# Kernel optimization log

Hardware: AMD Instinct MI355X
Metric: run time of the kernel (lower is better)

The kernel has to match this reference:

```python
import jax, jax.numpy as jnp
import numpy as np

E = 128  # embedding dim (edim)
NEG_INF = -1e8


def setup_inputs() -> dict:
    key = jax.random.key(0)
    ks = jax.random.split(key, 12)
    n_users, n_items, B, L = 100000, 50000, 4096, 64
    s = 1.0 / np.sqrt(2 * E)
    return {
        "user_embs": jax.random.normal(ks[0], (n_users, E), jnp.float32),
        "item_embs": jax.random.normal(ks[1], (n_items, E), jnp.float32),
        "w_uu": jax.random.normal(ks[2], (2 * E,), jnp.float32) * s,
        "w_uiu": jax.random.normal(ks[3], (2 * E,), jnp.float32) * s,
        "w_uui": jax.random.normal(ks[4], (2 * E,), jnp.float32) * s,
        "W0": jax.random.normal(ks[5], (E, E // 2), jnp.float32) / np.sqrt(E),
        "b0": jax.random.normal(ks[6], (E // 2,), jnp.float32) * 0.01,
        "w1": jax.random.normal(ks[7], (E // 2,), jnp.float32) / np.sqrt(E // 2),
        "uid": jax.random.randint(ks[8], (B,), 0, n_users),
        "nbr": jax.random.randint(ks[9], (B, L), 0, n_users),
        "uiu": jax.random.randint(ks[10], (B, 2, L), 0, n_items),
        "uui": jax.random.randint(ks[11], (B, 2, L), 0, n_items),
    }


def reference(user_embs, item_embs, w_uu, w_uiu, w_uui, W0, b0, w1, uid, nbr, uiu, uui):
    self_emb = user_embs[uid][:, None, :]  # [B,1,E]

    def branch(feat, mask, w):
        # feat: [B,L,E], mask: [B,L] bool. concat([self,feat]) @ w split into two GEMVs.
        logits = self_emb @ w[:E, None] + feat @ w[E:, None]  # [B,L,1]
        logits = jax.nn.leaky_relu(logits)  # slope 0.01, matches F.leaky_relu default
        logits = logits + NEG_INF * mask[:, :, None].astype(feat.dtype)
        a = jax.nn.softmax(logits, axis=1)  # over neighbor dim
        return jax.nn.relu(jnp.sum(a * feat, axis=1))  # [B,E]

    # uu meta-path
    uu_feat = branch((self_emb + user_embs[nbr]) * 0.5, nbr == 0, w_uu)
    # uiu meta-path: row 0 = item ids, row 1 = user ids
    mp_iid, mp_uid = uiu[:, 0], uiu[:, 1]
    uiu_feat = branch((self_emb + item_embs[mp_iid] + user_embs[mp_uid]) / 3.0, mp_iid == 0, w_uiu)
    # uui meta-path: row 0 = user ids, row 1 = item ids
    mp_uid2, mp_iid2 = uui[:, 0], uui[:, 1]
    uui_feat = branch((self_emb + user_embs[mp_uid2] + item_embs[mp_iid2]) / 3.0, mp_uid2 == 0, w_uui)

    def inter(feat):
        return jnp.tanh(feat @ W0 + b0).mean(axis=0) @ w1  # scalar

    scores = jnp.stack([inter(uu_feat), inter(uiu_feat), inter(uui_feat)])
    mp = jax.nn.softmax(scores)
    return jax.nn.relu(mp[0] * uu_feat + mp[1] * uiu_feat + mp[2] * uui_feat)
```

## Files before the change

kernel.cpp:

```cpp
#include <hip/hip_runtime.h>
#include <hip/hip_bf16.h>

#define E_DIM 128
#define L_DIM 64
#define HDIM 64

__device__ __forceinline__ float waveSum(float v) {
#pragma unroll
  for (int o = 32; o > 0; o >>= 1) v += __shfl_xor(v, o);
  return v;
}
__device__ __forceinline__ float waveMax(float v) {
#pragma unroll
  for (int o = 32; o > 0; o >>= 1) v = fmaxf(v, __shfl_xor(v, o));
  return v;
}
__device__ __forceinline__ float halfSum(float v) {
#pragma unroll
  for (int o = 16; o > 0; o >>= 1) v += __shfl_xor(v, o);
  return v;
}

__device__ __forceinline__ unsigned int f2bf(float f) {
  unsigned int u = __float_as_uint(f);
  return (u + 0x7fffu + ((u >> 16) & 1u)) >> 16;
}
__device__ __forceinline__ float lo_bf(unsigned int q) {
  return __uint_as_float(q << 16);
}
__device__ __forceinline__ float hi_bf(unsigned int q) {
  return __uint_as_float(q & 0xffff0000u);
}

__global__ __launch_bounds__(256) void convert_all(
    const float* __restrict__ user_src, const float* __restrict__ item_src,
    unsigned short* __restrict__ user_bf, unsigned short* __restrict__ item_bf,
    const float* __restrict__ w_uu, const float* __restrict__ w_uiu,
    const float* __restrict__ w_uui, float* __restrict__ pU0,
    float* __restrict__ pU1, float* __restrict__ pU2,
    float* __restrict__ pI1, float* __restrict__ pI2, int nUr, int nIr) {
  const int lane = threadIdx.x & 63;
  const int j = lane & 31;
  const int h = lane >> 5;
  const int gw = blockIdx.x * 4 + (threadIdx.x >> 6);
  const int r_all = gw * 2 + h;
  if (r_all >= nUr + nIr) return;

  const bool is_user = (r_all < nUr);
  const int r = is_user ? r_all : r_all - nUr;
  const float* src = is_user ? user_src : item_src;
  unsigned short* dst = is_user ? user_bf : item_bf;

  const float4 v = *(const float4*)(src + (long)r * E_DIM + j * 4);
  const unsigned int b0p = f2bf(v.x) | (f2bf(v.y) << 16);
  const unsigned int b1p = f2bf(v.z) | (f2bf(v.w) << 16);
  ((uint2*)dst)[(long)r * (E_DIM / 4) + j] = make_uint2(b0p, b1p);
  const float x0 = lo_bf(b0p), x1 = hi_bf(b0p);
  const float x2 = lo_bf(b1p), x3 = hi_bf(b1p);

  const float* wA = is_user ? w_uu : w_uiu;
  const float* wB = is_user ? w_uiu : w_uui;
  const float4 a4 = *(const float4*)(wA + E_DIM + j * 4);
  const float dA = halfSum(x0 * a4.x + x1 * a4.y + x2 * a4.z + x3 * a4.w);
  const float4 b4 = *(const float4*)(wB + E_DIM + j * 4);
  const float dB = halfSum(x0 * b4.x + x1 * b4.y + x2 * b4.z + x3 * b4.w);
  float dC = 0.f;
  if (is_user) {
    const float4 c4 = *(const float4*)(w_uui + E_DIM + j * 4);
    dC = halfSum(x0 * c4.x + x1 * c4.y + x2 * c4.z + x3 * c4.w);
  }
  if (j == 0) {
    if (is_user) {
      pU0[r] = dA;
      pU1[r] = dB;
      pU2[r] = dC;
    } else {
      pI1[r] = dA;
      pI2[r] = dB;
    }
  }
}

__global__ __launch_bounds__(256) void phase1_proj(
    const float* __restrict__ user_embs,
    const unsigned short* __restrict__ user_bf,
    const unsigned short* __restrict__ item_bf,
    const float* __restrict__ projU0, const float* __restrict__ projU1,
    const float* __restrict__ projU2, const float* __restrict__ projI1,
    const float* __restrict__ projI2,
    const float* __restrict__ w_uu, const float* __restrict__ w_uiu,
    const float* __restrict__ w_uui, const float* __restrict__ W0,
    const float* __restrict__ b0, const float* __restrict__ w1,
    const int* __restrict__ uid, const int* __restrict__ nbr,
    const int* __restrict__ uiu, const int* __restrict__ uui,
    float* __restrict__ feats,
    float* __restrict__ partials,
    int B) {
  const int lane = threadIdx.x & 63;
  const int j = lane & 15;
  const int quarter = lane >> 4;
  const int wv = threadIdx.x >> 6;
  const int w_id = blockIdx.x * 4 + wv;
  const int b = w_id / 3;
  const int k = w_id - 3 * b;
  if (b >= B) return;

  __shared__ float sc[4][E_DIM];

  const int u = uid[b];
  const float2 self2 = *(const float2*)(user_embs + (long)u * E_DIM + lane * 2);

  const float* w = (k == 0) ? w_uu : (k == 1) ? w_uiu : w_uui;
  const float2 wa = *(const float2*)(w + lane * 2);
  const float2 wb = *(const float2*)(w + E_DIM + lane * 2);
  const float S1 = waveSum(self2.x * wa.x + self2.y * wa.y);
  const float S2 = waveSum(self2.x * wb.x + self2.y * wb.y);

  const bool is_uu = (k == 0);
  const float scale = is_uu ? 0.5f : (1.0f / 3.0f);
  const uint4* T0 = (const uint4*)((k == 1) ? item_bf : user_bf);
  const uint4* T1 = (const uint4*)((k == 1) ? user_bf : item_bf);
  const float* p0 = (k == 0) ? projU0 : (k == 1) ? projI1 : projU2;
  const float* p1 = (k == 1) ? projU1 : projI2;

  int i0_l, i1_l;
  if (is_uu) {
    i0_l = nbr[b * L_DIM + lane];
    i1_l = 0;
  } else {
    const int* mp = (k == 1) ? uiu : uui;
    i0_l = mp[(b * 2 + 0) * L_DIM + lane];
    i1_l = mp[(b * 2 + 1) * L_DIM + lane];
  }

  float d = p0[i0_l];
  if (!is_uu) d += p1[i1_l];
  float logit = S1 + scale * (S2 + d);
  logit = (logit > 0.f) ? logit : 0.01f * logit;
  if (i0_l == 0) logit += -100000000.0f;

  const float M = waveMax(logit);
  const float p = __expf(logit - M);
  const float Z = waveSum(p);
  const float a_l = p / Z;

  constexpr int RQ = E_DIM / 8;
  float o0 = 0.f, o1 = 0.f, o2 = 0.f, o3 = 0.f;
  float o4 = 0.f, o5 = 0.f, o6 = 0.f, o7 = 0.f;

  int l4 = quarter;
  float a_cur = __shfl(a_l, l4);
  int i0 = __shfl(i0_l, l4);
  uint4 q0 = T0[(long)i0 * RQ + j];
  uint4 q1 = make_uint4(0, 0, 0, 0);
  if (!is_uu) {
    const int i1 = __shfl(i1_l, l4);
    q1 = T1[(long)i1 * RQ + j];
  }

  for (int it = 0; it < L_DIM / 4; ++it) {
    const float a = a_cur;
    const uint4 qa = q0;
    const uint4 qb = q1;
    if (it < L_DIM / 4 - 1) {
      l4 = 4 * (it + 1) + quarter;
      a_cur = __shfl(a_l, l4);
      i0 = __shfl(i0_l, l4);
      q0 = T0[(long)i0 * RQ + j];
      if (!is_uu) {
        const int i1 = __shfl(i1_l, l4);
        q1 = T1[(long)i1 * RQ + j];
      }
    }
    float h0 = lo_bf(qa.x), h1 = hi_bf(qa.x);
    float h2 = lo_bf(qa.y), h3 = hi_bf(qa.y);
    float h4 = lo_bf(qa.z), h5 = hi_bf(qa.z);
    float h6 = lo_bf(qa.w), h7 = hi_bf(qa.w);
    if (!is_uu) {
      h0 += lo_bf(qb.x); h1 += hi_bf(qb.x);
      h2 += lo_bf(qb.y); h3 += hi_bf(qb.y);
      h4 += lo_bf(qb.z); h5 += hi_bf(qb.z);
      h6 += lo_bf(qb.w); h7 += hi_bf(qb.w);
    }
    o0 += a * h0; o1 += a * h1; o2 += a * h2; o3 += a * h3;
    o4 += a * h4; o5 += a * h5; o6 += a * h6; o7 += a * h7;
  }
  o0 += __shfl_xor(o0, 16); o0 += __shfl_xor(o0, 32);
  o1 += __shfl_xor(o1, 16); o1 += __shfl_xor(o1, 32);
  o2 += __shfl_xor(o2, 16); o2 += __shfl_xor(o2, 32);
  o3 += __shfl_xor(o3, 16); o3 += __shfl_xor(o3, 32);
  o4 += __shfl_xor(o4, 16); o4 += __shfl_xor(o4, 32);
  o5 += __shfl_xor(o5, 16); o5 += __shfl_xor(o5, 32);
  o6 += __shfl_xor(o6, 16); o6 += __shfl_xor(o6, 32);
  o7 += __shfl_xor(o7, 16); o7 += __shfl_xor(o7, 32);

  const float4 sA = *(const float4*)(user_embs + (long)u * E_DIM + j * 8);
  const float4 sB = *(const float4*)(user_embs + (long)u * E_DIM + j * 8 + 4);
  float4 rA, rB;
  rA.x = fmaxf((sA.x + o0) * scale, 0.f);
  rA.y = fmaxf((sA.y + o1) * scale, 0.f);
  rA.z = fmaxf((sA.z + o2) * scale, 0.f);
  rA.w = fmaxf((sA.w + o3) * scale, 0.f);
  rB.x = fmaxf((sB.x + o4) * scale, 0.f);
  rB.y = fmaxf((sB.y + o5) * scale, 0.f);
  rB.z = fmaxf((sB.z + o6) * scale, 0.f);
  rB.w = fmaxf((sB.w + o7) * scale, 0.f);
  if (lane < 16) {
    float* fp = feats + ((long)k * B + b) * E_DIM + j * 8;
    *(float4*)fp = rA;
    *(float4*)(fp + 4) = rB;
    *(float4*)(&sc[wv][j * 8]) = rA;
    *(float4*)(&sc[wv][j * 8 + 4]) = rB;
  }
  __syncthreads();

  float hid = b0[lane];
#pragma unroll 4
  for (int e = 0; e < E_DIM; ++e) hid += sc[wv][e] * W0[e * HDIM + lane];
  const float pp = tanhf(hid) * w1[lane];
  const float sum = waveSum(pp);
  if (lane == 0) partials[(long)k * B + b] = sum;
}

__global__ __launch_bounds__(256) void phase1_f32(
    const float* __restrict__ user_embs, const float* __restrict__ item_embs,
    const float* __restrict__ w_uu, const float* __restrict__ w_uiu,
    const float* __restrict__ w_uui, const float* __restrict__ W0,
    const float* __restrict__ b0, const float* __restrict__ w1,
    const int* __restrict__ uid, const int* __restrict__ nbr,
    const int* __restrict__ uiu, const int* __restrict__ uui,
    float* __restrict__ feats, float* __restrict__ partials, int B) {
  const int lane = threadIdx.x & 63;
  const int wv = threadIdx.x >> 6;
  const int w_id = blockIdx.x * 4 + wv;
  const int b = w_id / 3;
  const int k = w_id - 3 * b;
  if (b >= B) return;

  __shared__ float sc[4][E_DIM];
  const int u = uid[b];
  const float self0 = user_embs[u * E_DIM + lane];
  const float self1 = user_embs[u * E_DIM + 64 + lane];
  const float* w = (k == 0) ? w_uu : (k == 1) ? w_uiu : w_uui;
  const float wa0 = w[lane], wa1 = w[64 + lane];
  const float wb0 = w[128 + lane], wb1 = w[192 + lane];
  const float logit_self = waveSum(self0 * wa0 + self1 * wa1);
  const bool is_uu = (k == 0);
  const float scale = is_uu ? 0.5f : (1.0f / 3.0f);
  const float* t0 = (k == 1) ? item_embs : user_embs;
  const float* t1 = (k == 1) ? user_embs : item_embs;
  int i0_l, i1_l;
  if (is_uu) {
    i0_l = nbr[b * L_DIM + lane];
    i1_l = 0;
  } else {
    const int* mp = (k == 1) ? uiu : uui;
    i0_l = mp[(b * 2 + 0) * L_DIM + lane];
    i1_l = mp[(b * 2 + 1) * L_DIM + lane];
  }
  const float mask_l = (i0_l == 0) ? 1.0f : 0.0f;
  float m = -3.0e38f, s = 0.0f, o0 = 0.0f, o1 = 0.0f;
  int i0 = __shfl(i0_l, 0), i1 = __shfl(i1_l, 0);
  float g00 = t0[i0 * E_DIM + lane];
  float g01 = t0[i0 * E_DIM + 64 + lane];
  float g10 = 0.f, g11 = 0.f;
  if (!is_uu) {
    g10 = t1[i1 * E_DIM + lane];
    g11 = t1[i1 * E_DIM + 64 + lane];
  }
  for (int l = 0; l < L_DIM; ++l) {
    const float f0 = (self0 + g00 + g10) * scale;
    const float f1 = (self1 + g01 + g11) * scale;
    if (l < L_DIM - 1) {
      i0 = __shfl(i0_l, l + 1);
      i1 = __shfl(i1_l, l + 1);
      g00 = t0[i0 * E_DIM + lane];
      g01 = t0[i0 * E_DIM + 64 + lane];
      if (!is_uu) {
        g10 = t1[i1 * E_DIM + lane];
        g11 = t1[i1 * E_DIM + 64 + lane];
      }
    }
    float logit = waveSum(f0 * wb0 + f1 * wb1) + logit_self;
    logit = (logit > 0.f) ? logit : 0.01f * logit;
    logit += -100000000.0f * __shfl(mask_l, l);
    const float mn = fmaxf(m, logit);
    const float alpha = __expf(m - mn);
    const float p = __expf(logit - mn);
    s = s * alpha + p;
    o0 = o0 * alpha + p * f0;
    o1 = o1 * alpha + p * f1;
    m = mn;
  }
  const float inv_s = 1.0f / s;
  const float r0 = fmaxf(o0 * inv_s, 0.f);
  const float r1 = fmaxf(o1 * inv_s, 0.f);
  feats[((long)k * B + b) * E_DIM + lane] = r0;
  feats[((long)k * B + b) * E_DIM + 64 + lane] = r1;
  sc[wv][lane] = r0;
  sc[wv][64 + lane] = r1;
  __syncthreads();
  float hid = b0[lane];
#pragma unroll 4
  for (int e = 0; e < E_DIM; ++e) hid += sc[wv][e] * W0[e * HDIM + lane];
  const float p = tanhf(hid) * w1[lane];
  const float sum = waveSum(p);
  if (lane == 0) partials[(long)k * B + b] = sum;
}

__global__ __launch_bounds__(256) void reduce_scores(
    const float* __restrict__ partials, float* __restrict__ weights, int B) {
  __shared__ float red[256];
  const int tid = threadIdx.x;
  float s[3];
#pragma unroll
  for (int k = 0; k < 3; ++k) {
    float acc = 0.f;
    for (int i = tid; i < B; i += 256) acc += partials[(long)k * B + i];
    red[tid] = acc;
    __syncthreads();
    for (int off = 128; off > 0; off >>= 1) {
      if (tid < off) red[tid] += red[tid + off];
      __syncthreads();
    }
    s[k] = red[0];
    __syncthreads();
  }
  if (tid == 0) {
    const float inv_b = 1.0f / (float)B;
    const float s0 = s[0] * inv_b, s1 = s[1] * inv_b, s2 = s[2] * inv_b;
    const float m = fmaxf(s0, fmaxf(s1, s2));
    const float e0 = __expf(s0 - m);
    const float e1 = __expf(s1 - m);
    const float e2 = __expf(s2 - m);
    const float inv = 1.0f / (e0 + e1 + e2);
    weights[0] = e0 * inv;
    weights[1] = e1 * inv;
    weights[2] = e2 * inv;
  }
}

__global__ __launch_bounds__(256) void phase2(
    const float* __restrict__ feats, const float* __restrict__ weights,
    float* __restrict__ out, int B) {
  const int i = blockIdx.x * blockDim.x + threadIdx.x;
  const int n = B * E_DIM;
  if (i >= n) return;
  const float w0 = weights[0], w1 = weights[1], w2 = weights[2];
  const float v = w0 * feats[i] + w1 * feats[n + i] + w2 * feats[2 * n + i];
  out[i] = fmaxf(v, 0.f);
}

__global__ __launch_bounds__(256) void phase2_fused(
    const float* __restrict__ partials, const float* __restrict__ feats,
    float* __restrict__ out, int B) {
  __shared__ float red[3][4];
  const int tid = threadIdx.x;
  const int lane = tid & 63;
  const int wv = tid >> 6;

  float s0 = 0.f, s1 = 0.f, s2 = 0.f;
  if ((B & 3) == 0) {
    const float4* p4 = (const float4*)partials;
    const int nb4 = B >> 2;
    for (int i = tid; i < nb4; i += 256) {
      const float4 v0 = p4[i];
      const float4 v1 = p4[nb4 + i];
      const float4 v2 = p4[2 * nb4 + i];
      s0 += (v0.x + v0.y) + (v0.z + v0.w);
      s1 += (v1.x + v1.y) + (v1.z + v1.w);
      s2 += (v2.x + v2.y) + (v2.z + v2.w);
    }
  } else {
    for (int i = tid; i < B; i += 256) {
      s0 += partials[i];
      s1 += partials[B + i];
      s2 += partials[2 * B + i];
    }
  }
  s0 = waveSum(s0);
  s1 = waveSum(s1);
  s2 = waveSum(s2);
  if (lane == 0) {
    red[0][wv] = s0;
    red[1][wv] = s1;
    red[2][wv] = s2;
  }
  __syncthreads();
  const float inv_b = 1.0f / (float)B;
  const float a0 = (red[0][0] + red[0][1] + red[0][2] + red[0][3]) * inv_b;
  const float a1 = (red[1][0] + red[1][1] + red[1][2] + red[1][3]) * inv_b;
  const float a2 = (red[2][0] + red[2][1] + red[2][2] + red[2][3]) * inv_b;
  const float m = fmaxf(a0, fmaxf(a1, a2));
  const float e0 = __expf(a0 - m);
  const float e1 = __expf(a1 - m);
  const float e2 = __expf(a2 - m);
  const float inv = 1.0f / (e0 + e1 + e2);
  const float w0 = e0 * inv, w1 = e1 * inv, w2 = e2 * inv;

  const int n4 = (B * E_DIM) >> 2;
  const float4* f4 = (const float4*)feats;
  float4* o4 = (float4*)out;
  for (int i = blockIdx.x * 256 + tid; i < n4; i += gridDim.x * 256) {
    const float4 x = f4[i];
    const float4 y = f4[n4 + i];
    const float4 z = f4[2 * n4 + i];
    float4 r;
    r.x = fmaxf(w0 * x.x + w1 * y.x + w2 * z.x, 0.f);
    r.y = fmaxf(w0 * x.y + w1 * y.y + w2 * z.y, 0.f);
    r.z = fmaxf(w0 * x.z + w1 * y.z + w2 * z.z, 0.f);
    r.w = fmaxf(w0 * x.w + w1 * y.w + w2 * z.w, 0.f);
    o4[i] = r;
  }
}

extern "C" void kernel_launch(void* const* d_in, const int* in_sizes, int n_in,
                              void* d_out, int out_size, void* d_ws,
                              size_t ws_size, hipStream_t stream) {
  const float* user_embs = (const float*)d_in[0];
  const float* item_embs = (const float*)d_in[1];
  const float* w_uu = (const float*)d_in[2];
  const float* w_uiu = (const float*)d_in[3];
  const float* w_uui = (const float*)d_in[4];
  const float* W0 = (const float*)d_in[5];
  const float* b0 = (const float*)d_in[6];
  const float* w1 = (const float*)d_in[7];
  const int* uid = (const int*)d_in[8];
  const int* nbr = (const int*)d_in[9];
  const int* uiu = (const int*)d_in[10];
  const int* uui = (const int*)d_in[11];
  const int B = in_sizes[8];
  const int nU = in_sizes[0];
  const int nI = in_sizes[1];
  const int nUr = nU / E_DIM;
  const int nIr = nI / E_DIM;

  float* ws = (float*)d_ws;
  float* partials = ws;
  float* weights = ws + 3 * B;
  float* feats = ws + 3 * B + 64;
  const size_t f32_floats = (size_t)3 * B + 64 + (size_t)3 * B * E_DIM;
  unsigned short* user_bf = (unsigned short*)(ws + f32_floats);
  unsigned short* item_bf = user_bf + nU;
  float* projU0 = (float*)(item_bf + nI);
  float* projU1 = projU0 + nUr;
  float* projU2 = projU1 + nUr;
  float* projI1 = projU2 + nUr;
  float* projI2 = projI1 + nIr;
  const size_t need = f32_floats * 4 + ((size_t)nU + nI) * 2 +
                      ((size_t)3 * nUr + 2 * nIr) * 4;

  const int n_waves = 3 * B;
  const int n_blocks = (n_waves + 3) / 4;
  const int n = B * E_DIM;

  if (ws_size >= need) {
    const int conv_waves = (nUr + nIr + 1) / 2;
    convert_all<<<(conv_waves + 3) / 4, 256, 0, stream>>>(
        user_embs, item_embs, user_bf, item_bf, w_uu, w_uiu, w_uui, projU0,
        projU1, projU2, projI1, projI2, nUr, nIr);
    phase1_proj<<<n_blocks, 256, 0, stream>>>(
        user_embs, user_bf, item_bf, projU0, projU1, projU2, projI1, projI2,
        w_uu, w_uiu, w_uui, W0, b0, w1, uid, nbr, uiu, uui, feats, partials,
        B);
    phase2_fused<<<256, 256, 0, stream>>>(partials, feats, (float*)d_out, B);
  } else {
    phase1_f32<<<n_blocks, 256, 0, stream>>>(user_embs, item_embs, w_uu,
                                             w_uiu, w_uui, W0, b0, w1, uid,
                                             nbr, uiu, uui, feats, partials, B);
    reduce_scores<<<1, 256, 0, stream>>>(partials, weights, B);
    phase2<<<(n + 255) / 256, 256, 0, stream>>>(feats, weights, (float*)d_out,
                                                B);
  }
}
```

Measured before the change: 203.0 us.

## Fuse convert, gather-attention and combine phases into one cooperative kernel

```diff
diff --git a/kernel.cpp b/kernel.cpp
--- a/kernel.cpp
+++ b/kernel.cpp
@@ -1,5 +1,8 @@
 #include <hip/hip_runtime.h>
 #include <hip/hip_bf16.h>
+#include <hip/hip_cooperative_groups.h>
+
+namespace cg = cooperative_groups;
 
 #define E_DIM 128
 #define L_DIM 64
@@ -30,6 +33,280 @@
 }
 __device__ __forceinline__ float hi_bf(unsigned int q) {
   return __uint_as_float(q & 0xffff0000u);
+}
+
+struct FusedArgs {
+  const float* user_embs;
+  const float* item_embs;
+  unsigned short* user_bf;
+  unsigned short* item_bf;
+  const float* w_uu;
+  const float* w_uiu;
+  const float* w_uui;
+  float* pU0;
+  float* pU1;
+  float* pU2;
+  float* pI1;
+  float* pI2;
+  const float* W0;
+  const float* b0;
+  const float* w1;
+  const int* uid;
+  const int* nbr;
+  const int* uiu;
+  const int* uui;
+  float* feats;
+  float* partials;
+  float* out;
+  int nUr;
+  int nIr;
+  int B;
+};
+
+__global__ __launch_bounds__(256) void fused_all(FusedArgs A) {
+  cg::grid_group grid = cg::this_grid();
+  const int lane = threadIdx.x & 63;
+  const int wv = threadIdx.x >> 6;
+
+  __shared__ float sc[4][E_DIM];
+  __shared__ float red[3][4];
+
+  {
+    const int j = lane & 31;
+    const int h = lane >> 5;
+    const int nRows = A.nUr + A.nIr;
+    const int wstride = gridDim.x * 4;
+    for (int gw = blockIdx.x * 4 + wv; gw * 2 < nRows; gw += wstride) {
+      const int r_all = gw * 2 + h;
+      if (r_all < nRows) {
+        const bool is_user = (r_all < A.nUr);
+        const int r = is_user ? r_all : r_all - A.nUr;
+        const float* src = is_user ? A.user_embs : A.item_embs;
+        unsigned short* dst = is_user ? A.user_bf : A.item_bf;
+
+        const float4 v = *(const float4*)(src + (long)r * E_DIM + j * 4);
+        const unsigned int b0p = f2bf(v.x) | (f2bf(v.y) << 16);
+        const unsigned int b1p = f2bf(v.z) | (f2bf(v.w) << 16);
+        ((uint2*)dst)[(long)r * (E_DIM / 4) + j] = make_uint2(b0p, b1p);
+        const float x0 = lo_bf(b0p), x1 = hi_bf(b0p);
+        const float x2 = lo_bf(b1p), x3 = hi_bf(b1p);
+
+        const float* wA = is_user ? A.w_uu : A.w_uiu;
+        const float* wB = is_user ? A.w_uiu : A.w_uui;
+        const float4 a4 = *(const float4*)(wA + E_DIM + j * 4);
+        const float dA = halfSum(x0 * a4.x + x1 * a4.y + x2 * a4.z + x3 * a4.w);
+        const float4 b4 = *(const float4*)(wB + E_DIM + j * 4);
+        const float dB = halfSum(x0 * b4.x + x1 * b4.y + x2 * b4.z + x3 * b4.w);
+        float dC = 0.f;
+        if (is_user) {
+          const float4 c4 = *(const float4*)(A.w_uui + E_DIM + j * 4);
+          dC = halfSum(x0 * c4.x + x1 * c4.y + x2 * c4.z + x3 * c4.w);
+        }
+        if (j == 0) {
+          if (is_user) {
+            A.pU0[r] = dA;
+            A.pU1[r] = dB;
+            A.pU2[r] = dC;
+          } else {
+            A.pI1[r] = dA;
+            A.pI2[r] = dB;
+          }
+        }
+      }
+    }
+  }
+  grid.sync();
+
+  {
+    const int j = lane & 15;
+    const int quarter = lane >> 4;
+    for (int base = blockIdx.x * 4; base < 3 * A.B; base += gridDim.x * 4) {
+      const int w_id = base + wv;
+      const bool valid = (w_id < 3 * A.B);
+      int b = 0, k = 0;
+      if (valid) {
+        b = w_id / 3;
+        k = w_id - 3 * b;
+
+        const int u = A.uid[b];
+        const float2 self2 =
+            *(const float2*)(A.user_embs + (long)u * E_DIM + lane * 2);
+
+        const float* w = (k == 0) ? A.w_uu : (k == 1) ? A.w_uiu : A.w_uui;
+        const float2 wa = *(const float2*)(w + lane * 2);
+        const float2 wb = *(const float2*)(w + E_DIM + lane * 2);
+        const float S1 = waveSum(self2.x * wa.x + self2.y * wa.y);
+        const float S2 = waveSum(self2.x * wb.x + self2.y * wb.y);
+
+        const bool is_uu = (k == 0);
+        const float scale = is_uu ? 0.5f : (1.0f / 3.0f);
+        const uint4* T0 = (const uint4*)((k == 1) ? A.item_bf : A.user_bf);
+        const uint4* T1 = (const uint4*)((k == 1) ? A.user_bf : A.item_bf);
+        const float* p0 = (k == 0) ? A.pU0 : (k == 1) ? A.pI1 : A.pU2;
+        const float* p1 = (k == 1) ? A.pU1 : A.pI2;
+
+        int i0_l, i1_l;
+        if (is_uu) {
+          i0_l = A.nbr[b * L_DIM + lane];
+          i1_l = 0;
+        } else {
+          const int* mp = (k == 1) ? A.uiu : A.uui;
+          i0_l = mp[(b * 2 + 0) * L_DIM + lane];
+          i1_l = mp[(b * 2 + 1) * L_DIM + lane];
+        }
+
+        float d = p0[i0_l];
+        if (!is_uu) d += p1[i1_l];
+        float logit = S1 + scale * (S2 + d);
+        logit = (logit > 0.f) ? logit : 0.01f * logit;
+        if (i0_l == 0) logit += -100000000.0f;
+
+        const float M = waveMax(logit);
+        const float p = __expf(logit - M);
+        const float Z = waveSum(p);
+        const float a_l = p / Z;
+
+        constexpr int RQ = E_DIM / 8;
+        float o0 = 0.f, o1 = 0.f, o2 = 0.f, o3 = 0.f;
+        float o4 = 0.f, o5 = 0.f, o6 = 0.f, o7 = 0.f;
+
+        int l4 = quarter;
+        float a_cur = __shfl(a_l, l4);
+        int i0 = __shfl(i0_l, l4);
+        uint4 q0 = T0[(long)i0 * RQ + j];
+        uint4 q1 = make_uint4(0, 0, 0, 0);
+        if (!is_uu) {
+          const int i1 = __shfl(i1_l, l4);
+          q1 = T1[(long)i1 * RQ + j];
+        }
+
+        for (int it = 0; it < L_DIM / 4; ++it) {
+          const float a = a_cur;
+          const uint4 qa = q0;
+          const uint4 qb = q1;
+          if (it < L_DIM / 4 - 1) {
+            l4 = 4 * (it + 1) + quarter;
+            a_cur = __shfl(a_l, l4);
+            i0 = __shfl(i0_l, l4);
+            q0 = T0[(long)i0 * RQ + j];
+            if (!is_uu) {
+              const int i1 = __shfl(i1_l, l4);
+              q1 = T1[(long)i1 * RQ + j];
+            }
+          }
+          float h0 = lo_bf(qa.x), h1 = hi_bf(qa.x);
+          float h2 = lo_bf(qa.y), h3 = hi_bf(qa.y);
+          float h4 = lo_bf(qa.z), h5 = hi_bf(qa.z);
+          float h6 = lo_bf(qa.w), h7 = hi_bf(qa.w);
+          if (!is_uu) {
+            h0 += lo_bf(qb.x); h1 += hi_bf(qb.x);
+            h2 += lo_bf(qb.y); h3 += hi_bf(qb.y);
+            h4 += lo_bf(qb.z); h5 += hi_bf(qb.z);
+            h6 += lo_bf(qb.w); h7 += hi_bf(qb.w);
+          }
+          o0 += a * h0; o1 += a * h1; o2 += a * h2; o3 += a * h3;
+          o4 += a * h4; o5 += a * h5; o6 += a * h6; o7 += a * h7;
+        }
+        o0 += __shfl_xor(o0, 16); o0 += __shfl_xor(o0, 32);
+        o1 += __shfl_xor(o1, 16); o1 += __shfl_xor(o1, 32);
+        o2 += __shfl_xor(o2, 16); o2 += __shfl_xor(o2, 32);
+        o3 += __shfl_xor(o3, 16); o3 += __shfl_xor(o3, 32);
+        o4 += __shfl_xor(o4, 16); o4 += __shfl_xor(o4, 32);
+        o5 += __shfl_xor(o5, 16); o5 += __shfl_xor(o5, 32);
+        o6 += __shfl_xor(o6, 16); o6 += __shfl_xor(o6, 32);
+        o7 += __shfl_xor(o7, 16); o7 += __shfl_xor(o7, 32);
+
+        const float4 sA =
+            *(const float4*)(A.user_embs + (long)u * E_DIM + j * 8);
+        const float4 sB =
+            *(const float4*)(A.user_embs + (long)u * E_DIM + j * 8 + 4);
+        float4 rA, rB;
+        rA.x = fmaxf((sA.x + o0) * scale, 0.f);
+        rA.y = fmaxf((sA.y + o1) * scale, 0.f);
+        rA.z = fmaxf((sA.z + o2) * scale, 0.f);
+        rA.w = fmaxf((sA.w + o3) * scale, 0.f);
+        rB.x = fmaxf((sB.x + o4) * scale, 0.f);
+        rB.y = fmaxf((sB.y + o5) * scale, 0.f);
+        rB.z = fmaxf((sB.z + o6) * scale, 0.f);
+        rB.w = fmaxf((sB.w + o7) * scale, 0.f);
+        if (lane < 16) {
+          float* fp = A.feats + ((long)k * A.B + b) * E_DIM + j * 8;
+          *(float4*)fp = rA;
+          *(float4*)(fp + 4) = rB;
+          *(float4*)(&sc[wv][j * 8]) = rA;
+          *(float4*)(&sc[wv][j * 8 + 4]) = rB;
+        }
+      }
+      __syncthreads();
+      if (valid) {
+        float hid = A.b0[lane];
+#pragma unroll 4
+        for (int e = 0; e < E_DIM; ++e) hid += sc[wv][e] * A.W0[e * HDIM + lane];
+        const float pp = tanhf(hid) * A.w1[lane];
+        const float sum = waveSum(pp);
+        if (lane == 0) A.partials[(long)k * A.B + b] = sum;
+      }
+      __syncthreads();
+    }
+  }
+  grid.sync();
+
+  {
+    const int tid = threadIdx.x;
+    float s0 = 0.f, s1 = 0.f, s2 = 0.f;
+    if ((A.B & 3) == 0) {
+      const float4* p4 = (const float4*)A.partials;
+      const int nb4 = A.B >> 2;
+      for (int i = tid; i < nb4; i += 256) {
+        const float4 v0 = p4[i];
+        const float4 v1 = p4[nb4 + i];
+        const float4 v2 = p4[2 * nb4 + i];
+        s0 += (v0.x + v0.y) + (v0.z + v0.w);
+        s1 += (v1.x + v1.y) + (v1.z + v1.w);
+        s2 += (v2.x + v2.y) + (v2.z + v2.w);
+      }
+    } else {
+      for (int i = tid; i < A.B; i += 256) {
+        s0 += A.partials[i];
+        s1 += A.partials[A.B + i];
+        s2 += A.partials[2 * A.B + i];
+      }
+    }
+    s0 = waveSum(s0);
+    s1 = waveSum(s1);
+    s2 = waveSum(s2);
+    if (lane == 0) {
+      red[0][wv] = s0;
+      red[1][wv] = s1;
+      red[2][wv] = s2;
+    }
+    __syncthreads();
+    const float inv_b = 1.0f / (float)A.B;
+    const float a0 = (red[0][0] + red[0][1] + red[0][2] + red[0][3]) * inv_b;
+    const float a1 = (red[1][0] + red[1][1] + red[1][2] + red[1][3]) * inv_b;
+    const float a2 = (red[2][0] + red[2][1] + red[2][2] + red[2][3]) * inv_b;
+    const float m = fmaxf(a0, fmaxf(a1, a2));
+    const float e0 = __expf(a0 - m);
+    const float e1 = __expf(a1 - m);
+    const float e2 = __expf(a2 - m);
+    const float inv = 1.0f / (e0 + e1 + e2);
+    const float w0 = e0 * inv, w1 = e1 * inv, w2 = e2 * inv;
+
+    const int n4 = (A.B * E_DIM) >> 2;
+    const float4* f4 = (const float4*)A.feats;
+    float4* o4 = (float4*)A.out;
+    for (int i = blockIdx.x * 256 + tid; i < n4; i += gridDim.x * 256) {
+      const float4 x = f4[i];
+      const float4 y = f4[n4 + i];
+      const float4 z = f4[2 * n4 + i];
+      float4 r;
+      r.x = fmaxf(w0 * x.x + w1 * y.x + w2 * z.x, 0.f);
+      r.y = fmaxf(w0 * x.y + w1 * y.y + w2 * z.y, 0.f);
+      r.z = fmaxf(w0 * x.z + w1 * y.z + w2 * z.z, 0.f);
+      r.w = fmaxf(w0 * x.w + w1 * y.w + w2 * z.w, 0.f);
+      o4[i] = r;
+    }
+  }
 }
 
 __global__ __launch_bounds__(256) void convert_all(
@@ -93,9 +370,7 @@
     const float* __restrict__ b0, const float* __restrict__ w1,
     const int* __restrict__ uid, const int* __restrict__ nbr,
     const int* __restrict__ uiu, const int* __restrict__ uui,
-    float* __restrict__ feats,
-    float* __restrict__ partials,
-    int B) {
+    float* __restrict__ feats, float* __restrict__ partials, int B) {
   const int lane = threadIdx.x & 63;
   const int j = lane & 15;
   const int quarter = lane >> 4;
@@ -455,15 +730,51 @@
   const int n = B * E_DIM;
 
   if (ws_size >= need) {
-    const int conv_waves = (nUr + nIr + 1) / 2;
-    convert_all<<<(conv_waves + 3) / 4, 256, 0, stream>>>(
-        user_embs, item_embs, user_bf, item_bf, w_uu, w_uiu, w_uui, projU0,
-        projU1, projU2, projI1, projI2, nUr, nIr);
-    phase1_proj<<<n_blocks, 256, 0, stream>>>(
-        user_embs, user_bf, item_bf, projU0, projU1, projU2, projI1, projI2,
-        w_uu, w_uiu, w_uui, W0, b0, w1, uid, nbr, uiu, uui, feats, partials,
-        B);
-    phase2_fused<<<256, 256, 0, stream>>>(partials, feats, (float*)d_out, B);
+    bool coop_done = false;
+    int dev = 0;
+    if (hipGetDevice(&dev) == hipSuccess) {
+      int coopAttr = 0, numCU = 0, perCU = 0;
+      hipDeviceGetAttribute(&coopAttr, hipDeviceAttributeCooperativeLaunch,
+                            dev);
+      hipDeviceGetAttribute(&numCU, hipDeviceAttributeMultiprocessorCount,
+                            dev);
+      hipError_t occErr =
+          hipOccupancyMaxActiveBlocksPerMultiprocessor(&perCU, fused_all, 256,
+                                                       0);
+      if (coopAttr && numCU > 0 && occErr == hipSuccess && perCU > 0) {
+        long grid = (long)perCU * numCU;
+        if (grid > 3072) grid = 3072;
+        FusedArgs fa;
+        fa.user_embs = user_embs; fa.item_embs = item_embs;
+        fa.user_bf = user_bf; fa.item_bf = item_bf;
+        fa.w_uu = w_uu; fa.w_uiu = w_uiu; fa.w_uui = w_uui;
+        fa.pU0 = projU0; fa.pU1 = projU1; fa.pU2 = projU2;
+        fa.pI1 = projI1; fa.pI2 = projI2;
+        fa.W0 = W0; fa.b0 = b0; fa.w1 = w1;
+        fa.uid = uid; fa.nbr = nbr; fa.uiu = uiu; fa.uui = uui;
+        fa.feats = feats; fa.partials = partials; fa.out = (float*)d_out;
+        fa.nUr = nUr; fa.nIr = nIr; fa.B = B;
+        void* kp[] = {&fa};
+        hipError_t e = hipLaunchCooperativeKernel(
+            fused_all, dim3((unsigned)grid), dim3(256), kp, 0, stream);
+        if (e == hipSuccess) {
+          coop_done = true;
+        } else {
+          (void)hipGetLastError();
+        }
+      }
+    }
+    if (!coop_done) {
+      const int conv_waves = (nUr + nIr + 1) / 2;
+      convert_all<<<(conv_waves + 3) / 4, 256, 0, stream>>>(
+          user_embs, item_embs, user_bf, item_bf, w_uu, w_uiu, w_uui, projU0,
+          projU1, projU2, projI1, projI2, nUr, nIr);
+      phase1_proj<<<n_blocks, 256, 0, stream>>>(
+          user_embs, user_bf, item_bf, projU0, projU1, projU2, projI1, projI2,
+          w_uu, w_uiu, w_uui, W0, b0, w1, uid, nbr, uiu, uui, feats, partials,
+          B);
+      phase2_fused<<<256, 256, 0, stream>>>(partials, feats, (float*)d_out, B);
+    }
   } else {
     phase1_f32<<<n_blocks, 256, 0, stream>>>(user_embs, item_embs, w_uu,
                                              w_uiu, w_uui, W0, b0, w1, uid,
```

After: 433.8 us. 2.14x slower.

## Quantize embedding tables to int8 with per-row scales for gather

Applied to the files above, without the earlier changes.

```diff
diff --git a/kernel.cpp b/kernel.cpp
--- a/kernel.cpp
+++ b/kernel.cpp
@@ -1,5 +1,4 @@
 #include <hip/hip_runtime.h>
-#include <hip/hip_bf16.h>
 
 #define E_DIM 128
 #define L_DIM 64
@@ -20,21 +19,17 @@
   for (int o = 16; o > 0; o >>= 1) v += __shfl_xor(v, o);
   return v;
 }
-
-__device__ __forceinline__ unsigned int f2bf(float f) {
-  unsigned int u = __float_as_uint(f);
-  return (u + 0x7fffu + ((u >> 16) & 1u)) >> 16;
-}
-__device__ __forceinline__ float lo_bf(unsigned int q) {
-  return __uint_as_float(q << 16);
-}
-__device__ __forceinline__ float hi_bf(unsigned int q) {
-  return __uint_as_float(q & 0xffff0000u);
-}
-
-__global__ __launch_bounds__(256) void convert_all(
+__device__ __forceinline__ float halfMax(float v) {
+#pragma unroll
+  for (int o = 16; o > 0; o >>= 1) v = fmaxf(v, __shfl_xor(v, o));
+  return v;
+}
+
+
+__global__ __launch_bounds__(256) void convert_i8(
     const float* __restrict__ user_src, const float* __restrict__ item_src,
-    unsigned short* __restrict__ user_bf, unsigned short* __restrict__ item_bf,
+    signed char* __restrict__ user_q, signed char* __restrict__ item_q,
+    float* __restrict__ user_s, float* __restrict__ item_s,
     const float* __restrict__ w_uu, const float* __restrict__ w_uiu,
     const float* __restrict__ w_uui, float* __restrict__ pU0,
     float* __restrict__ pU1, float* __restrict__ pU2,
@@ -49,42 +44,60 @@
   const bool is_user = (r_all < nUr);
   const int r = is_user ? r_all : r_all - nUr;
   const float* src = is_user ? user_src : item_src;
-  unsigned short* dst = is_user ? user_bf : item_bf;
+  signed char* dst = is_user ? user_q : item_q;
 
   const float4 v = *(const float4*)(src + (long)r * E_DIM + j * 4);
-  const unsigned int b0p = f2bf(v.x) | (f2bf(v.y) << 16);
-  const unsigned int b1p = f2bf(v.z) | (f2bf(v.w) << 16);
-  ((uint2*)dst)[(long)r * (E_DIM / 4) + j] = make_uint2(b0p, b1p);
-  const float x0 = lo_bf(b0p), x1 = hi_bf(b0p);
-  const float x2 = lo_bf(b1p), x3 = hi_bf(b1p);
+
+  float am =
+      fmaxf(fmaxf(fabsf(v.x), fabsf(v.y)), fmaxf(fabsf(v.z), fabsf(v.w)));
+  am = halfMax(am);
+  const float s = am * (1.0f / 127.0f);
+  const float inv = (am > 0.f) ? 127.0f / am : 0.f;
+
+  int q0 = __float2int_rn(v.x * inv);
+  int q1 = __float2int_rn(v.y * inv);
+  int q2 = __float2int_rn(v.z * inv);
+  int q3 = __float2int_rn(v.w * inv);
+  q0 = max(-127, min(127, q0));
+  q1 = max(-127, min(127, q1));
+  q2 = max(-127, min(127, q2));
+  q3 = max(-127, min(127, q3));
+  const unsigned int pk = (unsigned int)(q0 & 255) |
+                          ((unsigned int)(q1 & 255) << 8) |
+                          ((unsigned int)(q2 & 255) << 16) |
+                          ((unsigned int)(q3 & 255) << 24);
+  ((unsigned int*)dst)[(long)r * (E_DIM / 4) + j] = pk;
 
   const float* wA = is_user ? w_uu : w_uiu;
   const float* wB = is_user ? w_uiu : w_uui;
   const float4 a4 = *(const float4*)(wA + E_DIM + j * 4);
-  const float dA = halfSum(x0 * a4.x + x1 * a4.y + x2 * a4.z + x3 * a4.w);
+  const float dA = halfSum(v.x * a4.x + v.y * a4.y + v.z * a4.z + v.w * a4.w);
   const float4 b4 = *(const float4*)(wB + E_DIM + j * 4);
-  const float dB = halfSum(x0 * b4.x + x1 * b4.y + x2 * b4.z + x3 * b4.w);
+  const float dB = halfSum(v.x * b4.x + v.y * b4.y + v.z * b4.z + v.w * b4.w);
   float dC = 0.f;
   if (is_user) {
     const float4 c4 = *(const float4*)(w_uui + E_DIM + j * 4);
-    dC = halfSum(x0 * c4.x + x1 * c4.y + x2 * c4.z + x3 * c4.w);
+    dC = halfSum(v.x * c4.x + v.y * c4.y + v.z * c4.z + v.w * c4.w);
   }
   if (j == 0) {
     if (is_user) {
+      user_s[r] = s;
       pU0[r] = dA;
       pU1[r] = dB;
       pU2[r] = dC;
     } else {
+      item_s[r] = s;
       pI1[r] = dA;
       pI2[r] = dB;
     }
   }
 }
 
-__global__ __launch_bounds__(256) void phase1_proj(
+__global__ __launch_bounds__(256) void phase1_i8(
     const float* __restrict__ user_embs,
-    const unsigned short* __restrict__ user_bf,
-    const unsigned short* __restrict__ item_bf,
+    const signed char* __restrict__ user_q,
+    const signed char* __restrict__ item_q,
+    const float* __restrict__ user_s, const float* __restrict__ item_s,
     const float* __restrict__ projU0, const float* __restrict__ projU1,
     const float* __restrict__ projU2, const float* __restrict__ projI1,
     const float* __restrict__ projI2,
@@ -118,8 +131,10 @@
 
   const bool is_uu = (k == 0);
   const float scale = is_uu ? 0.5f : (1.0f / 3.0f);
-  const uint4* T0 = (const uint4*)((k == 1) ? item_bf : user_bf);
-  const uint4* T1 = (const uint4*)((k == 1) ? user_bf : item_bf);
+  const uint2* T0 = (const uint2*)((k == 1) ? item_q : user_q);
+  const uint2* T1 = (const uint2*)((k == 1) ? user_q : item_q);
+  const float* S0t = (k == 1) ? item_s : user_s;
+  const float* S1t = (k == 1) ? user_s : item_s;
   const float* p0 = (k == 0) ? projU0 : (k == 1) ? projI1 : projU2;
   const float* p1 = (k == 1) ? projU1 : projI2;
 
@@ -144,46 +159,57 @@
   const float Z = waveSum(p);
   const float a_l = p / Z;
 
+  const float as0_l = a_l * S0t[i0_l];
+  const float as1_l = is_uu ? 0.f : a_l * S1t[i1_l];
+
   constexpr int RQ = E_DIM / 8;
   float o0 = 0.f, o1 = 0.f, o2 = 0.f, o3 = 0.f;
   float o4 = 0.f, o5 = 0.f, o6 = 0.f, o7 = 0.f;
 
   int l4 = quarter;
-  float a_cur = __shfl(a_l, l4);
+  float a0c = __shfl(as0_l, l4);
+  float a1c = 0.f;
   int i0 = __shfl(i0_l, l4);
-  uint4 q0 = T0[(long)i0 * RQ + j];
-  uint4 q1 = make_uint4(0, 0, 0, 0);
+  uint2 q0 = T0[(long)i0 * RQ + j];
+  uint2 q1 = make_uint2(0, 0);
   if (!is_uu) {
+    a1c = __shfl(as1_l, l4);
     const int i1 = __shfl(i1_l, l4);
     q1 = T1[(long)i1 * RQ + j];
   }
 
   for (int it = 0; it < L_DIM / 4; ++it) {
-    const float a = a_cur;
-    const uint4 qa = q0;
-    const uint4 qb = q1;
+    const float a0 = a0c, a1 = a1c;
+    const uint2 qa = q0, qb = q1;
     if (it < L_DIM / 4 - 1) {
       l4 = 4 * (it + 1) + quarter;
-      a_cur = __shfl(a_l, l4);
+      a0c = __shfl(as0_l, l4);
       i0 = __shfl(i0_l, l4);
       q0 = T0[(long)i0 * RQ + j];
       if (!is_uu) {
+        a1c = __shfl(as1_l, l4);
         const int i1 = __shfl(i1_l, l4);
         q1 = T1[(long)i1 * RQ + j];
       }
     }
-    float h0 = lo_bf(qa.x), h1 = hi_bf(qa.x);
-    float h2 = lo_bf(qa.y), h3 = hi_bf(qa.y);
-    float h4 = lo_bf(qa.z), h5 = hi_bf(qa.z);
-    float h6 = lo_bf(qa.w), h7 = hi_bf(qa.w);
+    o0 += a0 * (float)(signed char)(qa.x);
+    o1 += a0 * (float)(signed char)(qa.x >> 8);
+    o2 += a0 * (float)(signed char)(qa.x >> 16);
+    o3 += a0 * (float)((int)qa.x >> 24);
+    o4 += a0 * (float)(signed char)(qa.y);
+    o5 += a0 * (float)(signed char)(qa.y >> 8);
+    o6 += a0 * (float)(signed char)(qa.y >> 16);
+    o7 += a0 * (float)((int)qa.y >> 24);
     if (!is_uu) {
-      h0 += lo_bf(qb.x); h1 += hi_bf(qb.x);
-      h2 += lo_bf(qb.y); h3 += hi_bf(qb.y);
-      h4 += lo_bf(qb.z); h5 += hi_bf(qb.z);
-      h6 += lo_bf(qb.w); h7 += hi_bf(qb.w);
-    }
-    o0 += a * h0; o1 += a * h1; o2 += a * h2; o3 += a * h3;
-    o4 += a * h4; o5 += a * h5; o6 += a * h6; o7 += a * h7;
+      o0 += a1 * (float)(signed char)(qb.x);
+      o1 += a1 * (float)(signed char)(qb.x >> 8);
+      o2 += a1 * (float)(signed char)(qb.x >> 16);
+      o3 += a1 * (float)((int)qb.x >> 24);
+      o4 += a1 * (float)(signed char)(qb.y);
+      o5 += a1 * (float)(signed char)(qb.y >> 8);
+      o6 += a1 * (float)(signed char)(qb.y >> 16);
+      o7 += a1 * (float)((int)qb.y >> 24);
+    }
   }
   o0 += __shfl_xor(o0, 16); o0 += __shfl_xor(o0, 32);
   o1 += __shfl_xor(o1, 16); o1 += __shfl_xor(o1, 32);
@@ -440,15 +466,20 @@
   float* weights = ws + 3 * B;
   float* feats = ws + 3 * B + 64;
   const size_t f32_floats = (size_t)3 * B + 64 + (size_t)3 * B * E_DIM;
-  unsigned short* user_bf = (unsigned short*)(ws + f32_floats);
-  unsigned short* item_bf = user_bf + nU;
-  float* projU0 = (float*)(item_bf + nI);
+  signed char* user_q = (signed char*)(ws + f32_floats);
+  signed char* item_q = user_q + nU;
+  const size_t qwords = ((size_t)nU + nI + 3) / 4;
+  float* user_s = ws + f32_floats + qwords;
+  float* item_s = user_s + nUr;
+  float* projU0 = item_s + nIr;
   float* projU1 = projU0 + nUr;
   float* projU2 = projU1 + nUr;
   float* projI1 = projU2 + nUr;
   float* projI2 = projI1 + nIr;
-  const size_t need = f32_floats * 4 + ((size_t)nU + nI) * 2 +
-                      ((size_t)3 * nUr + 2 * nIr) * 4;
+  const size_t need =
+      (f32_floats + qwords + (size_t)(nUr + nIr) + (size_t)3 * nUr +
+       (size_t)2 * nIr) *
+      4;
 
   const int n_waves = 3 * B;
   const int n_blocks = (n_waves + 3) / 4;
@@ -456,13 +487,13 @@
 
   if (ws_size >= need) {
     const int conv_waves = (nUr + nIr + 1) / 2;
-    convert_all<<<(conv_waves + 3) / 4, 256, 0, stream>>>(
-        user_embs, item_embs, user_bf, item_bf, w_uu, w_uiu, w_uui, projU0,
-        projU1, projU2, projI1, projI2, nUr, nIr);
-    phase1_proj<<<n_blocks, 256, 0, stream>>>(
-        user_embs, user_bf, item_bf, projU0, projU1, projU2, projI1, projI2,
-        w_uu, w_uiu, w_uui, W0, b0, w1, uid, nbr, uiu, uui, feats, partials,
-        B);
+    convert_i8<<<(conv_waves + 3) / 4, 256, 0, stream>>>(
+        user_embs, item_embs, user_q, item_q, user_s, item_s, w_uu, w_uiu,
+        w_uui, projU0, projU1, projU2, projI1, projI2, nUr, nIr);
+    phase1_i8<<<n_blocks, 256, 0, stream>>>(
+        user_embs, user_q, item_q, user_s, item_s, projU0, projU1, projU2,
+        projI1, projI2, w_uu, w_uiu, w_uui, W0, b0, w1, uid, nbr, uiu, uui,
+        feats, partials, B);
     phase2_fused<<<256, 256, 0, stream>>>(partials, feats, (float*)d_out, B);
   } else {
     phase1_f32<<<n_blocks, 256, 0, stream>>>(user_embs, item_embs, w_uu,
```

Result: faster. 188.2 us (-7.3%).
